# Performance work log

Hardware: AMD Instinct MI355X
Metric: run time of the kernel (lower is better)

Reference implementation:

```python
import jax, jax.numpy as jnp
import numpy as np
from math import factorial

MUL = 32                      # multiplicity of each node irrep: 32x0e + 32x1o + 32x2e
LS = (0, 1, 2)
DIMS = (1, 3, 5)
IN_DIM = MUL * sum(DIMS)      # 288
SH_DIM = sum(DIMS)            # 9  (1x0e + 1x1o + 1x2e)
RADIAL_DIM = 64
NUM_NEIGHBORS = 10.0
# FullyConnectedTensorProduct instructions (i_in, i_edge, i_out), e3nn enumeration order
INS = ((0, 0, 0), (0, 1, 1), (0, 2, 2), (1, 0, 1), (1, 1, 0), (1, 1, 2),
       (1, 2, 1), (2, 0, 2), (2, 1, 1), (2, 2, 0), (2, 2, 2))
N_PATHS = (3, 4, 4)           # number of paths feeding each output irrep
# e3nn 'component' irrep-norm + 'element' path-norm: path_weight = sqrt((2l_out+1)/sum_paths(mul1*mul2))
PW = tuple(((2 * l + 1) / (n * MUL)) ** 0.5 for l, n in zip(LS, N_PATHS))
WEIGHT_NUMEL = len(INS) * MUL * MUL   # 11264


def _su2_cg(j1, j2, j3):
    f = factorial
    C = np.zeros((2 * j1 + 1, 2 * j2 + 1, 2 * j3 + 1))
    for m1 in range(-j1, j1 + 1):
        for m2 in range(-j2, j2 + 1):
            m3 = m1 + m2
            if abs(m3) > j3:
                continue
            vmin = max(-j1 + j2 + m3, -j1 + m1, 0)
            vmax = min(j2 + j3 + m1, j3 - j1 + j2, j3 + m3)
            c = ((2 * j3 + 1) * f(j3 + j1 - j2) * f(j3 - j1 + j2) * f(j1 + j2 - j3)
                 * f(j3 + m3) * f(j3 - m3)
                 / (f(j1 + j2 + j3 + 1) * f(j1 - m1) * f(j1 + m1) * f(j2 - m2) * f(j2 + m2))) ** 0.5
            s = sum((-1) ** (v + j2 + m2) * f(j2 + j3 + m1 - v) * f(j1 - m1 + v)
                    / (f(v) * f(j3 - j1 + j2 - v) * f(j3 + m3 - v) * f(v + j1 - j2 - m3))
                    for v in range(vmin, vmax + 1))
            C[m1 + j1, m2 + j2, m3 + j3] = c * s
    return C


def _q_real_to_complex(l):
    q = np.zeros((2 * l + 1, 2 * l + 1), dtype=complex)
    for m in range(-l, 0):
        q[l + m, l + abs(m)] = 2 ** -0.5
        q[l + m, l - abs(m)] = -1j * 2 ** -0.5
    q[l, l] = 1.0
    for m in range(1, l + 1):
        q[l + m, l + abs(m)] = (-1) ** m * 2 ** -0.5
        q[l + m, l - abs(m)] = 1j * (-1) ** m * 2 ** -0.5
    return (-1j) ** l * q


def _wigner_3j(l1, l2, l3):
    C = _su2_cg(l1, l2, l3).astype(complex)
    Q1, Q2, Q3 = _q_real_to_complex(l1), _q_real_to_complex(l2), _q_real_to_complex(l3)
    C = np.real(np.einsum('ij,kl,mn,ikn->jlm', Q1, Q2, np.conj(Q3).T, C))
    return (C / np.linalg.norm(C)).astype(np.float32)  # e3nn convention: ||w3j||_F = 1


W3J = {ins: jnp.asarray(_wigner_3j(LS[ins[0]], LS[ins[1]], LS[ins[2]])) for ins in INS}

# e3nn normalize2mom constant for silu: 1/sqrt(E[silu(N(0,1))^2])
_z = np.random.RandomState(0).randn(1_000_000)
SILU_CST = float(1.0 / np.sqrt(np.mean((_z / (1.0 + np.exp(-_z))) ** 2)))
del _z


def _split_irreps(x, mul):
    blocks, off = [], 0
    for d in DIMS:
        blocks.append(x[:, off:off + mul * d].reshape(x.shape[0], mul, d))
        off += mul * d
    return blocks


def weight_nn(edge_radial, W1, W2):
    # e3nn FullyConnectedNet([64, 64, numel], silu): W/sqrt(fan_in), 2nd-moment-normalized act
    h = SILU_CST * jax.nn.silu(edge_radial @ (W1 / np.float32(RADIAL_DIM ** 0.5)))
    return h @ (W2 / np.float32(64 ** 0.5))


def tensor_product(x, sh, w):
    # per-edge FullyConnectedTensorProduct(irreps_in x irreps_edge -> irreps_out), shared_weights=False
    E = x.shape[0]
    xs = _split_irreps(x, MUL)        # [E, 32, 2l+1] per l
    shs = _split_irreps(sh, 1)        # [E, 1, 2l+1] per l
    outs = [jnp.zeros((E, MUL, d), x.dtype) for d in DIMS]
    off = 0
    for ins in INS:
        i1, i2, i3 = ins
        wi = w[:, off:off + MUL * MUL].reshape(E, MUL, MUL)  # (u, v=1, w) flattened
        off += MUL * MUL
        outs[i3] = outs[i3] + np.float32(PW[i3]) * jnp.einsum(
            'ijk,eui,ej,euw->ewk', W3J[ins], xs[i1], shs[i2][:, 0, :], wi)
    return jnp.concatenate([o.reshape(E, -1) for o in outs], axis=1)


def self_connection(x, Ws):
    # o3.Linear(irreps_in, irreps_out): per-irrep channel mixing, scaled by 1/sqrt(fan_in)
    blocks = _split_irreps(x, MUL)
    outs = [jnp.einsum('nud,uw->nwd', b, Wl / np.float32(MUL ** 0.5)).reshape(x.shape[0], -1)
            for b, Wl in zip(blocks, Ws)]
    return jnp.concatenate(outs, axis=1)


def _forward(node_features, edge_index, edge_sh, edge_radial, W1, W2, Wsc0, Wsc1, Wsc2):
    src, dst = edge_index[0], edge_index[1]
    n_nodes = node_features.shape[0]
    w = weight_nn(edge_radial, W1, W2)                          # [E, 11264]
    messages = tensor_product(node_features[src], edge_sh, w)   # [E, 288]
    agg = jnp.zeros((n_nodes, messages.shape[1]), messages.dtype).at[dst].add(messages)
    agg = agg / np.float32(NUM_NEIGHBORS ** 0.5)
    return agg + self_connection(node_features, (Wsc0, Wsc1, Wsc2))


def setup_inputs() -> dict:
    key = jax.random.key(0)
    ks = jax.random.split(key, 9)
    n_nodes, n_edges = 2000, 20000
    return {
        'node_features': jax.random.normal(ks[0], (n_nodes, IN_DIM), jnp.float32),
        'edge_index': jax.random.randint(ks[1], (2, n_edges), 0, n_nodes, jnp.int32),
        'edge_sh': jax.random.normal(ks[2], (n_edges, SH_DIM), jnp.float32),
        'edge_radial': jax.random.normal(ks[3], (n_edges, RADIAL_DIM), jnp.float32),
        'W1': jax.random.normal(ks[4], (RADIAL_DIM, 64), jnp.float32),
        'W2': jax.random.normal(ks[5], (64, WEIGHT_NUMEL), jnp.float32),
        'Wsc0': jax.random.normal(ks[6], (MUL, MUL), jnp.float32),
        'Wsc1': jax.random.normal(ks[7], (MUL, MUL), jnp.float32),
        'Wsc2': jax.random.normal(ks[8], (MUL, MUL), jnp.float32),
    }


def reference(node_features, edge_index, edge_sh, edge_radial, W1, W2, Wsc0, Wsc1, Wsc2):
    return _forward(node_features, edge_index, edge_sh, edge_radial, W1, W2, Wsc0, Wsc1, Wsc2)
```

## Files before the change

kernel.cpp:

```cpp
#include <hip/hip_runtime.h>
#include <math.h>

#define TILE_E 32
#define NINS 11
#define IND 288
#define SHD 9
#define W2N 11264
#define YROW 164
#define SHWP 28

typedef _Float16 half8 __attribute__((ext_vector_type(8)));
typedef float f32x4 __attribute__((ext_vector_type(4)));

constexpr int kL1[NINS] = {0,0,0,1,1,1,1,2,2,2,2};
constexpr int kL2[NINS] = {0,1,2,0,1,1,2,0,1,2,2};
constexpr int kL3[NINS] = {0,1,2,1,0,2,1,2,1,0,2};
constexpr int kW3OFF[NINS] = {0,1,10,35,44,53,98,143,168,213,238};

__device__ double dfac(int n){ double r=1.0; for(int i=2;i<=n;++i) r*=(double)i; return r; }

__device__ void qmat_dev(int l,double* qr,double* qi){
  int d=2*l+1;
  for(int i=0;i<d*d;++i){qr[i]=0.0;qi[i]=0.0;}
  const double s=0.70710678118654752440;
  for(int m=-l;m<0;++m){
    qr[(l+m)*d+(l-m)]=s;
    qi[(l+m)*d+(l+m)]=-s;
  }
  qr[l*d+l]=1.0;
  for(int m=1;m<=l;++m){
    double sg=(m&1)?-1.0:1.0;
    qr[(l+m)*d+(l+m)]=sg*s;
    qi[(l+m)*d+(l-m)]=sg*s;
  }
  if(l==1){ for(int i=0;i<d*d;++i){ double a=qr[i],b=qi[i]; qr[i]=b; qi[i]=-a; } }
  else if(l==2){ for(int i=0;i<d*d;++i){ qr[i]=-qr[i]; qi[i]=-qi[i]; } }
}

__device__ void w3j_body(int ins, int t, float* w3j){
  const int l1=kL1[ins],l2=kL2[ins],l3=kL3[ins];
  const int d1=2*l1+1,d2=2*l2+1,d3=2*l3+1;
  const int n=d1*d2*d3;

  __shared__ double C[125];
  __shared__ double R[125];
  __shared__ double q1r[25],q1i[25],q2r[25],q2i[25],q3r[25],q3i[25];
  __shared__ double inv;

  for(int i=t;i<125;i+=256) C[i]=0.0;
  if(t==0){
    qmat_dev(l1,q1r,q1i); qmat_dev(l2,q2r,q2i); qmat_dev(l3,q3r,q3i);
  }
  __syncthreads();

  if(t<d1*d2){
    int m1=t/d2-l1, m2=t-(t/d2)*d2-l2;
    int m3=m1+m2;
    if(m3>=-l3 && m3<=l3){
      int vmin=-l1+l2+m3; if(-l1+m1>vmin)vmin=-l1+m1; if(0>vmin)vmin=0;
      int vmax=l2+l3+m1; if(l3-l1+l2<vmax)vmax=l3-l1+l2; if(l3+m3<vmax)vmax=l3+m3;
      double c=sqrt((double)(2*l3+1)*dfac(l3+l1-l2)*dfac(l3-l1+l2)*dfac(l1+l2-l3)
        *dfac(l3+m3)*dfac(l3-m3)
        /(dfac(l1+l2+l3+1)*dfac(l1-m1)*dfac(l1+m1)*dfac(l2-m2)*dfac(l2+m2)));
      double s=0.0;
      for(int v=vmin;v<=vmax;++v){
        double term=dfac(l2+l3+m1-v)*dfac(l1-m1+v)
          /(dfac(v)*dfac(l3-l1+l2-v)*dfac(l3+m3-v)*dfac(v+l1-l2-m3));
        s += (((v+l2+m2)&1)?-1.0:1.0)*term;
      }
      C[((m1+l1)*d2+(m2+l2))*d3+(m3+l3)]=c*s;
    }
  }
  __syncthreads();

  if(t<n){
    int j=t/(d2*d3);
    int rem=t-j*(d2*d3);
    int l=rem/d3, m=rem-l*d3;
    double sr=0.0;
    for(int a=0;a<d1;++a)for(int b=0;b<d2;++b)for(int nn=0;nn<d3;++nn){
      double cv=C[(a*d2+b)*d3+nn];
      if(cv==0.0) continue;
      double xr=q1r[a*d1+j],xi=q1i[a*d1+j];
      double yr=q2r[b*d2+l],yi=q2i[b*d2+l];
      double zr=q3r[nn*d3+m],zi=-q3i[nn*d3+m];
      double pr=xr*yr-xi*yi, pi=xr*yi+xi*yr;
      sr += (pr*zr-pi*zi)*cv;
    }
    R[t]=sr;
  }
  __syncthreads();
  if(t==0){
    double n2=0.0;
    for(int i=0;i<n;++i) n2+=R[i]*R[i];
    inv=1.0/sqrt(n2);
  }
  __syncthreads();
  if(t<n) w3j[kW3OFF[ins]+t]=(float)(R[t]*inv);
}

__device__ void pack_body(int pb, int t, const float* __restrict__ W2,
                          _Float16* __restrict__ w2h){
  int q = pb*256 + t;
  if(q >= 704*2*64) return;
  int l = q & 63;
  int s = (q>>6)&1;
  int g = q>>7;
  int ins=g>>6, rem=g&63, uc=rem>>4, tp=rem&15;
  int m = l&15;
  int col = ins*1024 + (uc*8 + (m&7))*32 + tp*2 + (m>>3);
  int c0  = s*32 + ((l>>4)<<3);
  half8 v;
  #pragma unroll
  for(int i=0;i<8;++i) v[i] = (_Float16)W2[(size_t)(c0+i)*W2N + col];
  *(half8*)&w2h[(size_t)q*8] = v;
}

__device__ void h_body(int hb, int t, const float* __restrict__ radial,
    const float* __restrict__ W1, _Float16* __restrict__ h16g, int E, float silu_cst){
  int idx = hb*256 + t;
  int e = idx>>6, c = idx&63;
  if(e>=E) return;
  const float* rr = radial + (size_t)e*64;
  float acc=0.f;
  #pragma unroll 8
  for(int r=0;r<64;++r) acc += rr[r]*W1[r*64+c];
  acc*=0.125f;
  float hv = silu_cst*acc/(1.f+expf(-acc));
  h16g[idx]=(_Float16)hv;
}

__global__ __launch_bounds__(256) void prep_kernel(float* w3j,
    const float* __restrict__ W2, _Float16* __restrict__ w2h,
    const float* __restrict__ radial, const float* __restrict__ W1,
    _Float16* __restrict__ h16g, int E, float silu_cst){
  int b=blockIdx.x, t=threadIdx.x;
  if(b<NINS)           w3j_body(b, t, w3j);
  else if(b<NINS+352)  pack_body(b-NINS, t, W2, w2h);
  else                 h_body(b-NINS-352, t, radial, W1, h16g, E, silu_cst);
}

__global__ __launch_bounds__(1024) void csr_kernel(const int* __restrict__ eidx,
    int* __restrict__ rowptr, int* __restrict__ cur, int E, int n){
  __shared__ int deg[2048];
  __shared__ int buf[1024];
  int t=threadIdx.x;
  for(int i=t;i<2048;i+=1024) deg[i]=0;
  __syncthreads();
  for(int e=t;e<E;e+=1024) atomicAdd(&deg[eidx[E+e]],1);
  __syncthreads();
  int i0=2*t, i1=2*t+1;
  int a=(i0<n)?deg[i0]:0;
  int b=(i1<n)?deg[i1]:0;
  int p=a+b;
  buf[t]=p;
  __syncthreads();
  for(int off=1; off<1024; off<<=1){
    int v=buf[t];
    int add=(t>=off)?buf[t-off]:0;
    __syncthreads();
    buf[t]=v+add;
    __syncthreads();
  }
  int excl=buf[t]-p;
  if(i0<n){ rowptr[i0]=excl;   cur[i0]=excl; }
  if(i1<n){ rowptr[i1]=excl+a; cur[i1]=excl+a; }
  if(t==1023) rowptr[n]=buf[1023];
}

__global__ __launch_bounds__(256) void fill_kernel(const int* __restrict__ eidx,
    int* __restrict__ cursor, int* __restrict__ elist, int E){
  int e=blockIdx.x*256+threadIdx.x;
  if(e>=E) return;
  int d=eidx[E+e];
  int pos=atomicAdd(&cursor[d],1);
  elist[pos]=e;
}

__global__ __launch_bounds__(256) void gather_kernel(const float* __restrict__ msgbuf,
    const int* __restrict__ rowptr, const int* __restrict__ elist,
    const float* __restrict__ x,
    const float* __restrict__ W0, const float* __restrict__ W1s, const float* __restrict__ W2s,
    float* __restrict__ out, int n_nodes)
{
  int n=blockIdx.x;
  if(n>=n_nodes) return;
  int s0=rowptr[n], s1=rowptr[n+1];
  const float inv=0.17677669529663689f;
  for(int o=threadIdx.x; o<IND; o+=blockDim.x){
    float acc=0.f;
    for(int j=s0;j<s1;++j)
      acc += msgbuf[(size_t)elist[j]*IND + o];
    const float* W; int w,k,d,xo;
    if(o<32){W=W0; w=o; k=0; d=1; xo=0;}
    else if(o<128){int r=o-32; W=W1s; d=3; w=r/3; k=r-w*3; xo=32;}
    else {int r=o-128; W=W2s; d=5; w=r/5; k=r-w*5; xo=128;}
    float ssc=0.f;
    const float* xr=x+(size_t)n*IND+xo+k;
    for(int u=0;u<32;++u) ssc += xr[u*d]*W[u*32+w];
    out[(size_t)n*IND+o]=acc + ssc*inv;
  }
}

__global__ __launch_bounds__(256) void sc_kernel(const float* __restrict__ x,
  const float* __restrict__ W0, const float* __restrict__ W1s, const float* __restrict__ W2s,
  float* __restrict__ out, int n_nodes)
{
  int n=blockIdx.x;
  if(n>=n_nodes) return;
  const float inv=0.17677669529663689f;
  for(int o=threadIdx.x; o<IND; o+=blockDim.x){
    const float* W; int w,k,d,xo;
    if(o<32){W=W0; w=o; k=0; d=1; xo=0;}
    else if(o<128){int r=o-32; W=W1s; d=3; w=r/3; k=r-w*3; xo=32;}
    else {int r=o-128; W=W2s; d=5; w=r/5; k=r-w*5; xo=128;}
    float s=0.f;
    const float* xr=x+(size_t)n*IND+xo+k;
    for(int u=0;u<32;++u) s += xr[u*d]*W[u*32+w];
    out[(size_t)n*IND+o]=s*inv;
  }
}

template<int INS>
__device__ __forceinline__ void b1_step(const float* __restrict__ w3j,
    const float* __restrict__ sh, float (*shw)[SHWP], int t, int e0, int E)
{
  constexpr int L1v=kL1[INS], L2v=kL2[INS];
  constexpr int D1=2*L1v+1, D2=2*L2v+1, D3=2*kL3[INS]+1;
  constexpr int SO=(L2v==0)?0:(L2v==1?1:4);
  const float* w3=w3j+kW3OFF[INS];
  constexpr int NN=TILE_E*D1*D3;
  for(int idx=t; idx<NN; idx+=256){
    int e=idx/(D1*D3), r=idx-e*(D1*D3);
    int i=r/D3, k=r-i*D3;
    int eg=e0+e;
    float s=0.f;
    if(eg<E){
      #pragma unroll
      for(int j=0;j<D2;++j) s += w3[(i*D2+j)*D3+k]*sh[(size_t)eg*SHD+SO+j];
    }
    shw[e][r]=s;
  }
}

template<int INS>
__device__ __forceinline__ void b2_step(const float* __restrict__ x,
    const int* __restrict__ eidx, const float (*shw)[SHWP], float (*yb)[YROW],
    int t, int e0, int E)
{
  constexpr int L1v=kL1[INS];
  constexpr int D1=2*L1v+1, D3=2*kL3[INS]+1;
  constexpr int XO=(L1v==0)?0:(L1v==1?32:128);
  constexpr int NN=TILE_E*32*D3;
  for(int idx=t; idx<NN; idx+=256){
    int e=idx/(32*D3), r=idx-e*(32*D3);
    int k=r>>5, u=r&31;
    int eg=e0+e;
    float s=0.f;
    if(eg<E){
      int srn=eidx[eg];
      const float* xr=x+(size_t)srn*IND+XO+u*D1;
      #pragma unroll
      for(int i=0;i<D1;++i) s += shw[e][i*D3+k]*xr[i];
    }
    yb[e][k*32+u]=s;
  }
}

template<int INS, int ND3>
__device__ __forceinline__ void comp_step(const float (*yb)[YROW],
    const half8* __restrict__ w2p,
    half8 hb00, half8 hb01, half8 hb10, half8 hb11,
    int ln, int eA, int upb, int wv,
    float (&p0)[4*ND3], float (&p1)[4*ND3])
{
  constexpr int D3=2*kL3[INS]+1;
  static_assert(D3==ND3, "group/ins D3 mismatch");

  #pragma unroll 1
  for(int uc=0; uc<4; ++uc){
    const half8* bp = w2p + (size_t)((INS*4+uc)*16 + wv*4)*128 + ln;
    half8 af[8];
    #pragma unroll
    for(int q=0;q<4;++q){ af[2*q]=bp[q*128]; af[2*q+1]=bp[q*128+64]; }

    f32x4 yv0[ND3], yv1[ND3];
    #pragma unroll
    for(int k=0;k<ND3;++k){
      yv0[k]=*(const f32x4*)&yb[eA][k*32 + uc*8 + upb];
      yv1[k]=*(const f32x4*)&yb[16+eA][k*32 + uc*8 + upb];
    }

    f32x4 z; z[0]=0.f; z[1]=0.f; z[2]=0.f; z[3]=0.f;
    #pragma unroll
    for(int q=0;q<4;++q){
      f32x4 a0=__builtin_amdgcn_mfma_f32_16x16x32_f16(af[2*q],  hb00,z,0,0,0);
      a0      =__builtin_amdgcn_mfma_f32_16x16x32_f16(af[2*q+1],hb01,a0,0,0,0);
      #pragma unroll
      for(int k=0;k<ND3;++k)
        p0[q*ND3+k] += a0[0]*yv0[k][0]+a0[1]*yv0[k][1]+a0[2]*yv0[k][2]+a0[3]*yv0[k][3];
      f32x4 a1=__builtin_amdgcn_mfma_f32_16x16x32_f16(af[2*q],  hb10,z,0,0,0);
      a1      =__builtin_amdgcn_mfma_f32_16x16x32_f16(af[2*q+1],hb11,a1,0,0,0);
      #pragma unroll
      for(int k=0;k<ND3;++k)
        p1[q*ND3+k] += a1[0]*yv1[k][0]+a1[1]*yv1[k][1]+a1[2]*yv1[k][2]+a1[3]*yv1[k][3];
    }
  }
}

template<int ND3>
__device__ __forceinline__ void flush_set(float* __restrict__ out,
    float* __restrict__ msgbuf, int eg, int d, int E, int OO,
    float pw, int gA, int wsel, int wv, float (&pacc)[4*ND3])
{
  constexpr int KHI=(ND3+1)/2;
  #pragma unroll
  for(int q=0;q<4;++q){
    #pragma unroll
    for(int k=0;k<ND3;++k){
      float p = pacc[q*ND3+k] + __shfl_xor(pacc[q*ND3+k], 16, 64);
      bool mine = (gA&1) ? (k>=KHI) : (k<KHI);
      if(mine && eg<E){
        int w=(wv*4+q)*2+wsel;
        if(msgbuf) msgbuf[(size_t)eg*IND + OO + w*ND3 + k] = pw*p;
        else       atomicAdd(&out[(size_t)d*IND + OO + w*ND3 + k], pw*p);
      }
    }
  }
}

__global__ __launch_bounds__(256) void tp_kernel(
    const float* __restrict__ x, const int* __restrict__ eidx,
    const float* __restrict__ sh, const _Float16* __restrict__ h16g,
    const _Float16* __restrict__ w2h, const float* __restrict__ w3j,
    float* __restrict__ out, float* __restrict__ msgbuf,
    int E, float pwc0, float pwc1, float pwc2)
{
  __shared__ float shw[2][TILE_E][SHWP];
  __shared__ float ybuf[2][TILE_E][YROW];

  const int t=threadIdx.x;
  const int bid=blockIdx.x;
  const int etile=bid/3, g=bid-etile*3;
  const int e0=etile*TILE_E;

  const int ln=t&63, wv=t>>6;
  const int eA=ln&15, gA=ln>>4;
  const int upb=(gA&1)*4;
  const int wsel=gA>>1;
  const int eg0=e0+eA, eg1=e0+16+eA;

  const int d0 = (eg0<E)? eidx[E+eg0] : -1;
  const int d1 = (eg1<E)? eidx[E+eg1] : -1;

  half8 hb00,hb01,hb10,hb11;
  #pragma unroll
  for(int i=0;i<8;++i){
    hb00[i]=(_Float16)0.f; hb01[i]=(_Float16)0.f;
    hb10[i]=(_Float16)0.f; hb11[i]=(_Float16)0.f;
  }
  if(eg0<E){
    hb00=*(const half8*)&h16g[(size_t)eg0*64 + gA*8];
    hb01=*(const half8*)&h16g[(size_t)eg0*64 + 32 + gA*8];
  }
  if(eg1<E){
    hb10=*(const half8*)&h16g[(size_t)eg1*64 + gA*8];
    hb11=*(const half8*)&h16g[(size_t)eg1*64 + 32 + gA*8];
  }

  const half8* w2p=(const half8*)w2h;

  if(g==0){
    float p0[4]={}, p1[4]={};
    b1_step<0>(w3j,sh,shw[0],t,e0,E); __syncthreads();
    b2_step<0>(x,eidx,shw[0],ybuf[0],t,e0,E); b1_step<4>(w3j,sh,shw[1],t,e0,E); __syncthreads();
    comp_step<0,1>(ybuf[0],w2p,hb00,hb01,hb10,hb11,ln,eA,upb,wv,p0,p1);
    b2_step<4>(x,eidx,shw[1],ybuf[1],t,e0,E); b1_step<9>(w3j,sh,shw[0],t,e0,E); __syncthreads();
    comp_step<4,1>(ybuf[1],w2p,hb00,hb01,hb10,hb11,ln,eA,upb,wv,p0,p1);
    b2_step<9>(x,eidx,shw[0],ybuf[0],t,e0,E); __syncthreads();
    comp_step<9,1>(ybuf[0],w2p,hb00,hb01,hb10,hb11,ln,eA,upb,wv,p0,p1);
    flush_set<1>(out,msgbuf,eg0,d0,E,0,pwc0,gA,wsel,wv,p0);
    flush_set<1>(out,msgbuf,eg1,d1,E,0,pwc0,gA,wsel,wv,p1);
  } else if(g==1){
    float p0[12]={}, p1[12]={};
    b1_step<1>(w3j,sh,shw[0],t,e0,E); __syncthreads();
    b2_step<1>(x,eidx,shw[0],ybuf[0],t,e0,E); b1_step<3>(w3j,sh,shw[1],t,e0,E); __syncthreads();
    comp_step<1,3>(ybuf[0],w2p,hb00,hb01,hb10,hb11,ln,eA,upb,wv,p0,p1);
    b2_step<3>(x,eidx,shw[1],ybuf[1],t,e0,E); b1_step<6>(w3j,sh,shw[0],t,e0,E); __syncthreads();
    comp_step<3,3>(ybuf[1],w2p,hb00,hb01,hb10,hb11,ln,eA,upb,wv,p0,p1);
    b2_step<6>(x,eidx,shw[0],ybuf[0],t,e0,E); b1_step<8>(w3j,sh,shw[1],t,e0,E); __syncthreads();
    comp_step<6,3>(ybuf[0],w2p,hb00,hb01,hb10,hb11,ln,eA,upb,wv,p0,p1);
    b2_step<8>(x,eidx,shw[1],ybuf[1],t,e0,E); __syncthreads();
    comp_step<8,3>(ybuf[1],w2p,hb00,hb01,hb10,hb11,ln,eA,upb,wv,p0,p1);
    flush_set<3>(out,msgbuf,eg0,d0,E,32,pwc1,gA,wsel,wv,p0);
    flush_set<3>(out,msgbuf,eg1,d1,E,32,pwc1,gA,wsel,wv,p1);
  } else {
    float p0[20]={}, p1[20]={};
    b1_step<2>(w3j,sh,shw[0],t,e0,E); __syncthreads();
    b2_step<2>(x,eidx,shw[0],ybuf[0],t,e0,E); b1_step<5>(w3j,sh,shw[1],t,e0,E); __syncthreads();
    comp_step<2,5>(ybuf[0],w2p,hb00,hb01,hb10,hb11,ln,eA,upb,wv,p0,p1);
    b2_step<5>(x,eidx,shw[1],ybuf[1],t,e0,E); b1_step<7>(w3j,sh,shw[0],t,e0,E); __syncthreads();
    comp_step<5,5>(ybuf[1],w2p,hb00,hb01,hb10,hb11,ln,eA,upb,wv,p0,p1);
    b2_step<7>(x,eidx,shw[0],ybuf[0],t,e0,E); b1_step<10>(w3j,sh,shw[1],t,e0,E); __syncthreads();
    comp_step<7,5>(ybuf[0],w2p,hb00,hb01,hb10,hb11,ln,eA,upb,wv,p0,p1);
    b2_step<10>(x,eidx,shw[1],ybuf[1],t,e0,E); __syncthreads();
    comp_step<10,5>(ybuf[1],w2p,hb00,hb01,hb10,hb11,ln,eA,upb,wv,p0,p1);
    flush_set<5>(out,msgbuf,eg0,d0,E,128,pwc2,gA,wsel,wv,p0);
    flush_set<5>(out,msgbuf,eg1,d1,E,128,pwc2,gA,wsel,wv,p1);
  }
}

extern "C" void kernel_launch(void* const* d_in, const int* in_sizes, int n_in,
                              void* d_out, int out_size, void* d_ws, size_t ws_size,
                              hipStream_t stream){
  const float* x     =(const float*)d_in[0];
  const int*   eidx  =(const int*)  d_in[1];
  const float* sh    =(const float*)d_in[2];
  const float* radial=(const float*)d_in[3];
  const float* W1    =(const float*)d_in[4];
  const float* W2    =(const float*)d_in[5];
  const float* Wsc0  =(const float*)d_in[6];
  const float* Wsc1  =(const float*)d_in[7];
  const float* Wsc2  =(const float*)d_in[8];
  float* out=(float*)d_out;
  int n_nodes=in_sizes[0]/IND;
  int E=in_sizes[1]/2;

  float inv10=1.0f/sqrtf(10.0f);
  float pwc0=sqrtf(1.0f/96.0f) *0.125f*inv10;
  float pwc1=sqrtf(3.0f/128.0f)*0.125f*inv10;
  float pwc2=sqrtf(5.0f/128.0f)*0.125f*inv10;
  float silu_cst=1.67682f;

  size_t off=0;
  auto alloc=[&](size_t bytes)->size_t{ size_t o=off; off=(off+bytes+255)&~(size_t)255; return o; };
  size_t o_w3j = alloc(2048);
  size_t o_w2h = alloc((size_t)704*2*64*8*2);
  size_t o_h16 = alloc((size_t)E*64*2);
  size_t o_row = alloc((size_t)(n_nodes+64)*4);
  size_t o_cur = alloc((size_t)(n_nodes+64)*4);
  size_t o_eli = alloc((size_t)E*4);
  size_t o_msg = alloc((size_t)E*IND*4);
  bool use_msg = (off <= ws_size) && (n_nodes < 2048);

  char* ws=(char*)d_ws;
  float*     w3j =(float*)(ws+o_w3j);
  _Float16*  w2h =(_Float16*)(ws+o_w2h);
  _Float16*  h16g=(_Float16*)(ws+o_h16);
  int*       row =(int*)(ws+o_row);
  int*       cur =(int*)(ws+o_cur);
  int*       eli =(int*)(ws+o_eli);
  float*     msg =(float*)(ws+o_msg);

  int ntile=(E+TILE_E-1)/TILE_E;
  int hblocks=(E*64+255)/256;

  hipLaunchKernelGGL(prep_kernel, dim3(NINS+352+hblocks), dim3(256), 0, stream,
                     w3j, W2, w2h, radial, W1, h16g, E, silu_cst);

  if(use_msg){
    hipLaunchKernelGGL(csr_kernel, dim3(1), dim3(1024), 0, stream, eidx, row, cur, E, n_nodes);
    hipLaunchKernelGGL(fill_kernel, dim3((E+255)/256), dim3(256), 0, stream, eidx, cur, eli, E);
    hipLaunchKernelGGL(tp_kernel, dim3(3*ntile), dim3(256), 0, stream,
                       x, eidx, sh, h16g, w2h, w3j, out, msg, E, pwc0, pwc1, pwc2);
    hipLaunchKernelGGL(gather_kernel, dim3(n_nodes), dim3(256), 0, stream,
                       msg, row, eli, x, Wsc0, Wsc1, Wsc2, out, n_nodes);
  } else {
    hipLaunchKernelGGL(sc_kernel, dim3(n_nodes), dim3(256), 0, stream,
                       x, Wsc0, Wsc1, Wsc2, out, n_nodes);
    hipLaunchKernelGGL(tp_kernel, dim3(3*ntile), dim3(256), 0, stream,
                       x, eidx, sh, h16g, w2h, w3j, out, (float*)nullptr, E, pwc0, pwc1, pwc2);
  }
}
```

Before: 228.0 us.

## Halve edge tile to 16 and fold CSR build into prep kernel

The edge tile per tensor-product block shrinks from 32 to 16 edges, so each wave runs one MFMA chain per step instead of two. That doubles the block count and frees registers and LDS for more occupancy, but the W2 fragments are reused across fewer edges. The single-block CSR construction moves out of its own 1024-thread kernel into an extra 256-thread block of the prep kernel, removing one launch and letting it overlap with the other prep work. The n_nodes bound is relaxed to <=2048.

Result: faster. 199.2 us (-12.6%).

```diff
diff --git a/kernel.cpp b/kernel.cpp
--- a/kernel.cpp
+++ b/kernel.cpp
@@ -1,7 +1,7 @@
 #include <hip/hip_runtime.h>
 #include <math.h>
 
-#define TILE_E 32
+#define TILE_E 16
 #define NINS 11
 #define IND 288
 #define SHD 9
@@ -130,42 +130,47 @@
   h16g[idx]=(_Float16)hv;
 }
 
+__device__ void csr_body(int t, const int* __restrict__ eidx,
+    int* __restrict__ rowptr, int* __restrict__ cur, int E, int n){
+  __shared__ int deg[2048];
+  __shared__ int psum[256];
+  for(int i=t;i<2048;i+=256) deg[i]=0;
+  __syncthreads();
+  for(int e=t;e<E;e+=256) atomicAdd(&deg[eidx[E+e]],1);
+  __syncthreads();
+  int base=t*8;
+  int loc[8]; int s=0;
+  #pragma unroll
+  for(int i=0;i<8;++i){ loc[i]=(base+i<n)?deg[base+i]:0; s+=loc[i]; }
+  psum[t]=s;
+  __syncthreads();
+  for(int off=1; off<256; off<<=1){
+    int v=psum[t];
+    int add=(t>=off)?psum[t-off]:0;
+    __syncthreads();
+    psum[t]=v+add;
+    __syncthreads();
+  }
+  int excl=psum[t]-s;
+  #pragma unroll
+  for(int i=0;i<8;++i){
+    if(base+i<n){ rowptr[base+i]=excl; cur[base+i]=excl; }
+    excl+=loc[i];
+  }
+  if(t==255) rowptr[n]=psum[255];
+}
+
 __global__ __launch_bounds__(256) void prep_kernel(float* w3j,
     const float* __restrict__ W2, _Float16* __restrict__ w2h,
     const float* __restrict__ radial, const float* __restrict__ W1,
-    _Float16* __restrict__ h16g, int E, float silu_cst){
+    _Float16* __restrict__ h16g, int E, float silu_cst,
+    const int* __restrict__ eidx, int* __restrict__ rowptr, int* __restrict__ cur,
+    int n_nodes, int hblocks){
   int b=blockIdx.x, t=threadIdx.x;
-  if(b<NINS)           w3j_body(b, t, w3j);
-  else if(b<NINS+352)  pack_body(b-NINS, t, W2, w2h);
-  else                 h_body(b-NINS-352, t, radial, W1, h16g, E, silu_cst);
-}
-
-__global__ __launch_bounds__(1024) void csr_kernel(const int* __restrict__ eidx,
-    int* __restrict__ rowptr, int* __restrict__ cur, int E, int n){
-  __shared__ int deg[2048];
-  __shared__ int buf[1024];
-  int t=threadIdx.x;
-  for(int i=t;i<2048;i+=1024) deg[i]=0;
-  __syncthreads();
-  for(int e=t;e<E;e+=1024) atomicAdd(&deg[eidx[E+e]],1);
-  __syncthreads();
-  int i0=2*t, i1=2*t+1;
-  int a=(i0<n)?deg[i0]:0;
-  int b=(i1<n)?deg[i1]:0;
-  int p=a+b;
-  buf[t]=p;
-  __syncthreads();
-  for(int off=1; off<1024; off<<=1){
-    int v=buf[t];
-    int add=(t>=off)?buf[t-off]:0;
-    __syncthreads();
-    buf[t]=v+add;
-    __syncthreads();
-  }
-  int excl=buf[t]-p;
-  if(i0<n){ rowptr[i0]=excl;   cur[i0]=excl; }
-  if(i1<n){ rowptr[i1]=excl+a; cur[i1]=excl+a; }
-  if(t==1023) rowptr[n]=buf[1023];
+  if(b<NINS)                  w3j_body(b, t, w3j);
+  else if(b<NINS+352)         pack_body(b-NINS, t, W2, w2h);
+  else if(b<NINS+352+hblocks) h_body(b-NINS-352, t, radial, W1, h16g, E, silu_cst);
+  else                        csr_body(t, eidx, rowptr, cur, E, n_nodes);
 }
 
 __global__ __launch_bounds__(256) void fill_kernel(const int* __restrict__ eidx,
@@ -270,9 +275,9 @@
 template<int INS, int ND3>
 __device__ __forceinline__ void comp_step(const float (*yb)[YROW],
     const half8* __restrict__ w2p,
-    half8 hb00, half8 hb01, half8 hb10, half8 hb11,
+    half8 hb0, half8 hb1,
     int ln, int eA, int upb, int wv,
-    float (&p0)[4*ND3], float (&p1)[4*ND3])
+    float (&p0)[4*ND3])
 {
   constexpr int D3=2*kL3[INS]+1;
   static_assert(D3==ND3, "group/ins D3 mismatch");
@@ -284,26 +289,19 @@
     #pragma unroll
     for(int q=0;q<4;++q){ af[2*q]=bp[q*128]; af[2*q+1]=bp[q*128+64]; }
 
-    f32x4 yv0[ND3], yv1[ND3];
+    f32x4 yv0[ND3];
     #pragma unroll
-    for(int k=0;k<ND3;++k){
+    for(int k=0;k<ND3;++k)
       yv0[k]=*(const f32x4*)&yb[eA][k*32 + uc*8 + upb];
-      yv1[k]=*(const f32x4*)&yb[16+eA][k*32 + uc*8 + upb];
-    }
 
     f32x4 z; z[0]=0.f; z[1]=0.f; z[2]=0.f; z[3]=0.f;
     #pragma unroll
     for(int q=0;q<4;++q){
-      f32x4 a0=__builtin_amdgcn_mfma_f32_16x16x32_f16(af[2*q],  hb00,z,0,0,0);
-      a0      =__builtin_amdgcn_mfma_f32_16x16x32_f16(af[2*q+1],hb01,a0,0,0,0);
+      f32x4 a0=__builtin_amdgcn_mfma_f32_16x16x32_f16(af[2*q],  hb0,z,0,0,0);
+      a0      =__builtin_amdgcn_mfma_f32_16x16x32_f16(af[2*q+1],hb1,a0,0,0,0);
       #pragma unroll
       for(int k=0;k<ND3;++k)
         p0[q*ND3+k] += a0[0]*yv0[k][0]+a0[1]*yv0[k][1]+a0[2]*yv0[k][2]+a0[3]*yv0[k][3];
-      f32x4 a1=__builtin_amdgcn_mfma_f32_16x16x32_f16(af[2*q],  hb10,z,0,0,0);
-      a1      =__builtin_amdgcn_mfma_f32_16x16x32_f16(af[2*q+1],hb11,a1,0,0,0);
-      #pragma unroll
-      for(int k=0;k<ND3;++k)
-        p1[q*ND3+k] += a1[0]*yv1[k][0]+a1[1]*yv1[k][1]+a1[2]*yv1[k][2]+a1[3]*yv1[k][3];
     }
   }
 }
@@ -348,65 +346,54 @@
   const int eA=ln&15, gA=ln>>4;
   const int upb=(gA&1)*4;
   const int wsel=gA>>1;
-  const int eg0=e0+eA, eg1=e0+16+eA;
+  const int eg0=e0+eA;
 
   const int d0 = (eg0<E)? eidx[E+eg0] : -1;
-  const int d1 = (eg1<E)? eidx[E+eg1] : -1;
-
-  half8 hb00,hb01,hb10,hb11;
+
+  half8 hb0, hb1;
   #pragma unroll
-  for(int i=0;i<8;++i){
-    hb00[i]=(_Float16)0.f; hb01[i]=(_Float16)0.f;
-    hb10[i]=(_Float16)0.f; hb11[i]=(_Float16)0.f;
-  }
+  for(int i=0;i<8;++i){ hb0[i]=(_Float16)0.f; hb1[i]=(_Float16)0.f; }
   if(eg0<E){
-    hb00=*(const half8*)&h16g[(size_t)eg0*64 + gA*8];
-    hb01=*(const half8*)&h16g[(size_t)eg0*64 + 32 + gA*8];
-  }
-  if(eg1<E){
-    hb10=*(const half8*)&h16g[(size_t)eg1*64 + gA*8];
-    hb11=*(const half8*)&h16g[(size_t)eg1*64 + 32 + gA*8];
+    hb0=*(const half8*)&h16g[(size_t)eg0*64 + gA*8];
+    hb1=*(const half8*)&h16g[(size_t)eg0*64 + 32 + gA*8];
   }
 
   const half8* w2p=(const half8*)w2h;
 
   if(g==0){
-    float p0[4]={}, p1[4]={};
+    float p0[4]={};
     b1_step<0>(w3j,sh,shw[0],t,e0,E); __syncthreads();
     b2_step<0>(x,eidx,shw[0],ybuf[0],t,e0,E); b1_step<4>(w3j,sh,shw[1],t,e0,E); __syncthreads();
-    comp_step<0,1>(ybuf[0],w2p,hb00,hb01,hb10,hb11,ln,eA,upb,wv,p0,p1);
+    comp_step<0,1>(ybuf[0],w2p,hb0,hb1,ln,eA,upb,wv,p0);
     b2_step<4>(x,eidx,shw[1],ybuf[1],t,e0,E); b1_step<9>(w3j,sh,shw[0],t,e0,E); __syncthreads();
-    comp_step<4,1>(ybuf[1],w2p,hb00,hb01,hb10,hb11,ln,eA,upb,wv,p0,p1);
+    comp_step<4,1>(ybuf[1],w2p,hb0,hb1,ln,eA,upb,wv,p0);
     b2_step<9>(x,eidx,shw[0],ybuf[0],t,e0,E); __syncthreads();
-    comp_step<9,1>(ybuf[0],w2p,hb00,hb01,hb10,hb11,ln,eA,upb,wv,p0,p1);
+    comp_step<9,1>(ybuf[0],w2p,hb0,hb1,ln,eA,upb,wv,p0);
     flush_set<1>(out,msgbuf,eg0,d0,E,0,pwc0,gA,wsel,wv,p0);
-    flush_set<1>(out,msgbuf,eg1,d1,E,0,pwc0,gA,wsel,wv,p1);
   } else if(g==1){
-    float p0[12]={}, p1[12]={};
+    float p0[12]={};
     b1_step<1>(w3j,sh,shw[0],t,e0,E); __syncthreads();
     b2_step<1>(x,eidx,shw[0],ybuf[0],t,e0,E); b1_step<3>(w3j,sh,shw[1],t,e0,E); __syncthreads();
-    comp_step<1,3>(ybuf[0],w2p,hb00,hb01,hb10,hb11,ln,eA,upb,wv,p0,p1);
+    comp_step<1,3>(ybuf[0],w2p,hb0,hb1,ln,eA,upb,wv,p0);
     b2_step<3>(x,eidx,shw[1],ybuf[1],t,e0,E); b1_step<6>(w3j,sh,shw[0],t,e0,E); __syncthreads();
-    comp_step<3,3>(ybuf[1],w2p,hb00,hb01,hb10,hb11,ln,eA,upb,wv,p0,p1);
+    comp_step<3,3>(ybuf[1],w2p,hb0,hb1,ln,eA,upb,wv,p0);
     b2_step<6>(x,eidx,shw[0],ybuf[0],t,e0,E); b1_step<8>(w3j,sh,shw[1],t,e0,E); __syncthreads();
-    comp_step<6,3>(ybuf[0],w2p,hb00,hb01,hb10,hb11,ln,eA,upb,wv,p0,p1);
+    comp_step<6,3>(ybuf[0],w2p,hb0,hb1,ln,eA,upb,wv,p0);
     b2_step<8>(x,eidx,shw[1],ybuf[1],t,e0,E); __syncthreads();
-    comp_step<8,3>(ybuf[1],w2p,hb00,hb01,hb10,hb11,ln,eA,upb,wv,p0,p1);
+    comp_step<8,3>(ybuf[1],w2p,hb0,hb1,ln,eA,upb,wv,p0);
     flush_set<3>(out,msgbuf,eg0,d0,E,32,pwc1,gA,wsel,wv,p0);
-    flush_set<3>(out,msgbuf,eg1,d1,E,32,pwc1,gA,wsel,wv,p1);
   } else {
-    float p0[20]={}, p1[20]={};
+    float p0[20]={};
     b1_step<2>(w3j,sh,shw[0],t,e0,E); __syncthreads();
     b2_step<2>(x,eidx,shw[0],ybuf[0],t,e0,E); b1_step<5>(w3j,sh,shw[1],t,e0,E); __syncthreads();
-    comp_step<2,5>(ybuf[0],w2p,hb00,hb01,hb10,hb11,ln,eA,upb,wv,p0,p1);
+    comp_step<2,5>(ybuf[0],w2p,hb0,hb1,ln,eA,upb,wv,p0);
     b2_step<5>(x,eidx,shw[1],ybuf[1],t,e0,E); b1_step<7>(w3j,sh,shw[0],t,e0,E); __syncthreads();
-    comp_step<5,5>(ybuf[1],w2p,hb00,hb01,hb10,hb11,ln,eA,upb,wv,p0,p1);
+    comp_step<5,5>(ybuf[1],w2p,hb0,hb1,ln,eA,upb,wv,p0);
     b2_step<7>(x,eidx,shw[0],ybuf[0],t,e0,E); b1_step<10>(w3j,sh,shw[1],t,e0,E); __syncthreads();
-    comp_step<7,5>(ybuf[0],w2p,hb00,hb01,hb10,hb11,ln,eA,upb,wv,p0,p1);
+    comp_step<7,5>(ybuf[0],w2p,hb0,hb1,ln,eA,upb,wv,p0);
     b2_step<10>(x,eidx,shw[1],ybuf[1],t,e0,E); __syncthreads();
-    comp_step<10,5>(ybuf[1],w2p,hb00,hb01,hb10,hb11,ln,eA,upb,wv,p0,p1);
+    comp_step<10,5>(ybuf[1],w2p,hb0,hb1,ln,eA,upb,wv,p0);
     flush_set<5>(out,msgbuf,eg0,d0,E,128,pwc2,gA,wsel,wv,p0);
-    flush_set<5>(out,msgbuf,eg1,d1,E,128,pwc2,gA,wsel,wv,p1);
   }
 }
 
@@ -441,7 +428,7 @@
   size_t o_cur = alloc((size_t)(n_nodes+64)*4);
   size_t o_eli = alloc((size_t)E*4);
   size_t o_msg = alloc((size_t)E*IND*4);
-  bool use_msg = (off <= ws_size) && (n_nodes < 2048);
+  bool use_msg = (off <= ws_size) && (n_nodes <= 2048);
 
   char* ws=(char*)d_ws;
   float*     w3j =(float*)(ws+o_w3j);
@@ -454,12 +441,13 @@
 
   int ntile=(E+TILE_E-1)/TILE_E;
   int hblocks=(E*64+255)/256;
-
-  hipLaunchKernelGGL(prep_kernel, dim3(NINS+352+hblocks), dim3(256), 0, stream,
-                     w3j, W2, w2h, radial, W1, h16g, E, silu_cst);
+  int prep_blocks = NINS+352+hblocks + (use_msg?1:0);
+
+  hipLaunchKernelGGL(prep_kernel, dim3(prep_blocks), dim3(256), 0, stream,
+                     w3j, W2, w2h, radial, W1, h16g, E, silu_cst,
+                     eidx, row, cur, n_nodes, hblocks);
 
   if(use_msg){
-    hipLaunchKernelGGL(csr_kernel, dim3(1), dim3(1024), 0, stream, eidx, row, cur, E, n_nodes);
     hipLaunchKernelGGL(fill_kernel, dim3((E+255)/256), dim3(256), 0, stream, eidx, cur, eli, E);
     hipLaunchKernelGGL(tp_kernel, dim3(3*ntile), dim3(256), 0, stream,
                        x, eidx, sh, h16g, w2h, w3j, out, msg, E, pwc0, pwc1, pwc2);
```
